# Performance work log

Hardware: AMD Instinct MI355X
Metric: run time of the kernel (lower is better)

## Reference

```python
import jax, jax.numpy as jnp
import numpy as np

N = 100000      # nodes per batched graph
E = 3200000     # edges per batched graph
G = 1024        # number of graphs in the batch
F_IN = 128
H = 64


def gcn_conv(x, src, dst, W, b, n):
    # PyG GCNConv: lin -> symmetric-normalized propagate (with self-loops) -> +bias
    xw = x @ W                                   # [n, out]
    deg = jnp.zeros((n,), x.dtype).at[dst].add(1.0) + 1.0   # A+I degree
    dinv = jax.lax.rsqrt(deg)                    # deg >= 1, safe
    norm = (dinv[src] * dinv[dst])[:, None]      # [E,1]
    agg = jax.ops.segment_sum(norm * xw[src], dst, num_segments=n)
    # self-loop contribution: dinv[i]^2 * xw[i]
    return agg + (dinv * dinv)[:, None] * xw + b


def mean_pool(h, batch, num_graphs):
    sums = jax.ops.segment_sum(h, batch, num_segments=num_graphs)
    cnt = jax.ops.segment_sum(jnp.ones((h.shape[0],), h.dtype), batch, num_segments=num_graphs)
    return sums / jnp.maximum(cnt, 1.0)[:, None]


def branch(x, edge_index, batch, W1, b1, W2, b2):
    src, dst = edge_index[0], edge_index[1]
    h = jax.nn.relu(gcn_conv(x, src, dst, W1, b1, x.shape[0]))
    h = jax.nn.relu(gcn_conv(h, src, dst, W2, b2, x.shape[0]))
    return mean_pool(h, batch, G)


def setup_inputs() -> dict:
    key = jax.random.key(0)
    ks = jax.random.split(key, 14)
    x1 = jax.random.normal(ks[0], (N, F_IN), jnp.float32)
    x2 = jax.random.normal(ks[1], (N, F_IN), jnp.float32)
    edge_index1 = jax.random.randint(ks[2], (2, E), 0, N, jnp.int32)
    edge_index2 = jax.random.randint(ks[3], (2, E), 0, N, jnp.int32)
    batch1 = jnp.sort(jax.random.randint(ks[4], (N,), 0, G, jnp.int32))
    batch2 = jnp.sort(jax.random.randint(ks[5], (N,), 0, G, jnp.int32))
    s = 1.0 / np.sqrt(F_IN)
    W1 = jax.random.uniform(ks[6], (F_IN, H), jnp.float32, -s, s)
    b1 = jnp.zeros((H,), jnp.float32)
    s2 = 1.0 / np.sqrt(H)
    W2 = jax.random.uniform(ks[7], (H, H), jnp.float32, -s2, s2)
    b2 = jnp.zeros((H,), jnp.float32)
    s3 = 1.0 / np.sqrt(3 * H)
    fc1_W = jax.random.uniform(ks[8], (3 * H, H), jnp.float32, -s3, s3)
    fc1_b = jax.random.uniform(ks[9], (H,), jnp.float32, -s3, s3)
    fc2_W = jax.random.uniform(ks[10], (H, 1), jnp.float32, -s2, s2)
    fc2_b = jax.random.uniform(ks[11], (1,), jnp.float32, -s2, s2)
    return {"x1": x1, "edge_index1": edge_index1, "batch1": batch1,
            "x2": x2, "edge_index2": edge_index2, "batch2": batch2,
            "W1": W1, "b1": b1, "W2": W2, "b2": b2,
            "fc1_W": fc1_W, "fc1_b": fc1_b, "fc2_W": fc2_W, "fc2_b": fc2_b}


def reference(x1, edge_index1, batch1, x2, edge_index2, batch2,
              W1, b1, W2, b2, fc1_W, fc1_b, fc2_W, fc2_b):
    emb1 = branch(x1, edge_index1, batch1, W1, b1, W2, b2)   # [G, 64]
    emb2 = branch(x2, edge_index2, batch2, W1, b1, W2, b2)   # [G, 64]
    combined = jnp.concatenate([emb1, emb2, jnp.abs(emb1 - emb2)], axis=1)  # [G, 192]
    out = jax.nn.relu(combined @ fc1_W + fc1_b)
    out = jax.nn.sigmoid(out @ fc2_W + fc2_b)
    return out.squeeze(-1)  # [G]
```

## Files before the change

kernel.cpp:

```cpp
#include <hip/hip_runtime.h>
#include <hip/hip_fp16.h>
#include <cstdint>


#define NBSH 8
#define CAPB 10240
#define SPLIT_T 512
#define SPLIT_EPT 28
#define SPLIT_CHUNK (SPLIT_T * SPLIT_EPT)

__device__ __forceinline__ float fatomic(float* p, float v) {
    return unsafeAtomicAdd(p, v);
}
__device__ __forceinline__ float bf2f(unsigned short u) {
    union { unsigned int i; float f; } c; c.i = ((unsigned int)u) << 16; return c.f;
}
__device__ __forceinline__ unsigned short f2bf(float f) {
    union { float f; unsigned int i; } c; c.f = f;
    const unsigned int b = c.i;
    return (unsigned short)((b + 0x7FFF + ((b >> 16) & 1)) >> 16);
}

#if defined(__has_builtin)
#if __has_builtin(__builtin_amdgcn_cvt_f32_fp8) && __has_builtin(__builtin_amdgcn_cvt_pk_fp8_f32)
#define HW_FP8 1
#endif
#endif

__device__ __forceinline__ float fp8dec(unsigned int b) {
#ifdef HW_FP8
    return __builtin_amdgcn_cvt_f32_fp8((int)b, 0);
#else
    const unsigned int mag = (b & 0x7Fu) << 20;
    const float f = __uint_as_float(mag) * __uint_as_float(0x7B800000u);
    const unsigned int r = __float_as_uint(f) | ((b & 0x80u) << 24);
    return __uint_as_float(r);
#endif
}

__device__ __forceinline__ unsigned char fp8enc(float x) {
#ifdef HW_FP8
    const int v = __builtin_amdgcn_cvt_pk_fp8_f32(x, x, 0, false);
    return (unsigned char)(v & 0xFF);
#else
    const unsigned short h = __half_as_ushort(__float2half(x));
    const unsigned int s = (unsigned int)(h >> 15) << 7;
    const int e = (h >> 10) & 0x1F;
    const unsigned int m = h & 0x3FFu;
    if (e == 31) return (unsigned char)(s | 0x7E);
    if (e == 0) return (unsigned char)s;
    int E = e - 15 + 7;
    if (E >= 16) return (unsigned char)(s | 0x7E);
    if (E <= 0) {
        const unsigned int M = 0x400u | m;
        const int r = 16 - e;
        const unsigned int q = (M + (1u << (r - 1)) - 1u + ((M >> r) & 1u)) >> r;
        return (unsigned char)(s | (q > 7u ? 8u : q));
    }
    unsigned int q = (m + 63u + ((m >> 7) & 1u)) >> 7;
    if (q == 8u) { q = 0u; ++E; if (E >= 16) return (unsigned char)(s | 0x7E); }
    return (unsigned char)(s | ((unsigned int)E << 3) | q);
#endif
}

__global__ __launch_bounds__(512) void k_split(const int* __restrict__ src,
                                               const int* __restrict__ dst,
                                               int* __restrict__ gcnt,
                                               int* __restrict__ colBkt,
                                               int E, int NBUK) {
    __shared__ int out[SPLIT_CHUNK];
    __shared__ int bs[513];
    __shared__ int aux[512];
    const int t = threadIdx.x;
    const int e0 = blockIdx.x * SPLIT_CHUNK;

    int pk[SPLIT_EPT];
    int bk[SPLIT_EPT];

    aux[t] = 0;
    __syncthreads();

#pragma unroll
    for (int k = 0; k < SPLIT_EPT; ++k) {
        const int e = e0 + t + SPLIT_T * k;
        if (e < E) {
            const int d = dst[e];
            const int s = src[e];
            const int b = d >> NBSH;
            pk[k] = (s << NBSH) | (d & ((1 << NBSH) - 1));
            bk[k] = b;
            atomicAdd(&aux[b], 1);
        } else {
            bk[k] = -1;
        }
    }
    __syncthreads();

    for (int off = 1; off < 512; off <<= 1) {
        const int u = (t >= off) ? aux[t - off] : 0;
        __syncthreads();
        aux[t] += u;
        __syncthreads();
    }
    bs[t + 1] = aux[t];
    if (t == 0) bs[0] = 0;
    __syncthreads();

    aux[t] = 0;
    __syncthreads();

#pragma unroll
    for (int k = 0; k < SPLIT_EPT; ++k) {
        if (bk[k] >= 0) {
            const int pos = bs[bk[k]] + atomicAdd(&aux[bk[k]], 1);
            out[pos] = pk[k];
        }
    }
    __syncthreads();

    if (t < NBUK) {
        const int L = bs[t + 1] - bs[t];
        aux[t] = (L > 0) ? atomicAdd(&gcnt[t], L) : 0;
    } else if (t < 512) {
        aux[t] = 0;
    }
    __syncthreads();

    const int wid = t >> 6, lane = t & 63;
    for (int b = wid; b < NBUK; b += 8) {
        const int L = bs[b + 1] - bs[b];
        if (L == 0) continue;
        const int gp = aux[b];
        const size_t rb = (size_t)b * CAPB;
        for (int k = lane; k < L; k += 64) {
            const int p = gp + k;
            if (p < CAPB) colBkt[rb + p] = out[bs[b] + k];
        }
    }
}

__global__ __launch_bounds__(512) void k_gscan(const int* __restrict__ gcnt,
                                               int* __restrict__ gbase,
                                               int* __restrict__ rowstart,
                                               int NBUK, int Nn) {
    __shared__ int sm[512];
    const int t = threadIdx.x;
    const int v = (t < NBUK) ? min(gcnt[t], CAPB) : 0;
    sm[t] = v;
    __syncthreads();
    for (int off = 1; off < 512; off <<= 1) {
        const int u = (t >= off) ? sm[t - off] : 0;
        __syncthreads();
        sm[t] += u;
        __syncthreads();
    }
    if (t < NBUK) gbase[t] = sm[t] - v;
    if (t == 511) rowstart[Nn] = sm[511];
}

__global__ __launch_bounds__(256) void k_bsort(const int* __restrict__ colBkt,
                                               const int* __restrict__ gcnt,
                                               const int* __restrict__ gbase,
                                               int* __restrict__ colN,
                                               int* __restrict__ rowstart,
                                               float* __restrict__ dinv,
                                               int Nn) {
    __shared__ int in[CAPB];
    __shared__ int lb[257];
    __shared__ int fill[256];
    const int b = blockIdx.x;
    const int t = threadIdx.x;
    const int L = min(gcnt[b], CAPB);
    const size_t rb = (size_t)b * CAPB;
    for (int k = t; k < L; k += 256) in[k] = colBkt[rb + k];
    fill[t] = 0;
    __syncthreads();
    for (int k = t; k < L; k += 256) atomicAdd(&fill[in[k] & 255], 1);
    __syncthreads();
    for (int off = 1; off < 256; off <<= 1) {
        const int u = (t >= off) ? fill[t - off] : 0;
        __syncthreads();
        fill[t] += u;
        __syncthreads();
    }
    lb[t + 1] = fill[t];
    if (t == 0) lb[0] = 0;
    __syncthreads();
    const int bb = gbase[b];
    const int node = (b << NBSH) + t;
    if (node < Nn) {
        rowstart[node] = bb + lb[t];
        dinv[node] = rsqrtf((float)(lb[t + 1] - lb[t]) + 1.0f);
    }
    fill[t] = 0;
    __syncthreads();
    for (int k = t; k < L; k += 256) {
        const int v = in[k];
        const int n = v & 255;
        const int pos = bb + lb[n] + atomicAdd(&fill[n], 1);
        colN[pos] = v >> NBSH;
    }
}

template <int K, bool BF16IN>
__global__ __launch_bounds__(256, 4) void k_mm(const void* __restrict__ Xv,
                                               const float* __restrict__ W,
                                               const float* __restrict__ dinv,
                                               unsigned char* __restrict__ Y, int n) {
    __shared__ float WL[K * 64];
    __shared__ float XT[32 * K];
    const int tid = threadIdx.x;
    for (int i = tid * 4; i < K * 64; i += 1024)
        *(float4*)&WL[i] = *(const float4*)&W[i];
    const int rowBase = blockIdx.x * 32;
    const int rows = min(32, n - rowBase);
    if (BF16IN) {
        const unsigned short* xs = (const unsigned short*)Xv + (size_t)rowBase * K;
        for (int i = tid * 4; i < rows * K; i += 1024) {
            const ushort4 u = *(const ushort4*)&xs[i];
            XT[i + 0] = bf2f(u.x); XT[i + 1] = bf2f(u.y);
            XT[i + 2] = bf2f(u.z); XT[i + 3] = bf2f(u.w);
        }
    } else {
        const float* xs = (const float*)Xv + (size_t)rowBase * K;
        for (int i = tid * 4; i < rows * K; i += 1024)
            *(float4*)&XT[i] = *(const float4*)&xs[i];
    }
    __syncthreads();
    const int colf = tid & 63;
    const int rg = tid >> 6;
    float acc[8] = {};
#pragma unroll 4
    for (int k4 = 0; k4 < K / 4; ++k4) {
        const float w0 = WL[(k4 * 4 + 0) * 64 + colf];
        const float w1 = WL[(k4 * 4 + 1) * 64 + colf];
        const float w2 = WL[(k4 * 4 + 2) * 64 + colf];
        const float w3 = WL[(k4 * 4 + 3) * 64 + colf];
#pragma unroll
        for (int r = 0; r < 8; ++r) {
            const float4 xv = *(const float4*)&XT[(rg * 8 + r) * K + k4 * 4];
            acc[r] += xv.x * w0 + xv.y * w1 + xv.z * w2 + xv.w * w3;
        }
    }
#pragma unroll
    for (int r = 0; r < 8; ++r) {
        const int row = rowBase + rg * 8 + r;
        if (row < n)
            __builtin_nontemporal_store(fp8enc(dinv[row] * acc[r]),
                                        &Y[(size_t)row * 64 + colf]);
    }
}

template <bool POOL>
__global__ __launch_bounds__(256) void k_agg(const int* __restrict__ colN,
                                             const int* __restrict__ rowstart,
                                             const float* __restrict__ dinv,
                                             const unsigned char* __restrict__ XW8,
                                             const float* __restrict__ bias,
                                             unsigned short* __restrict__ Hout,
                                             const int* __restrict__ batch,
                                             float* __restrict__ emb,
                                             float* __restrict__ cnt, int Nn) {
    const int lane = threadIdx.x & 63;
    const int wid = (blockIdx.x * blockDim.x + threadIdx.x) >> 6;
    const int nw = (gridDim.x * blockDim.x) >> 6;
    const float bl = bias[lane];
    for (int i = wid; i < Nn; i += nw) {
        const int s = rowstart[i], e = rowstart[i + 1];
        float acc = 0.0f;
        int j = s;
        for (; j + 16 <= e; j += 16) {
            int c[16];
#pragma unroll
            for (int q = 0; q < 16; ++q) c[q] = __builtin_nontemporal_load(&colN[j + q]);
            unsigned int b[16];
#pragma unroll
            for (int q = 0; q < 16; ++q) b[q] = XW8[(size_t)c[q] * 64 + lane];
            float t0 = 0.f, t1 = 0.f;
#pragma unroll
            for (int q = 0; q < 8; ++q) t0 += fp8dec(b[q]);
#pragma unroll
            for (int q = 8; q < 16; ++q) t1 += fp8dec(b[q]);
            acc += t0 + t1;
        }
        for (; j + 4 <= e; j += 4) {
            const int c0 = __builtin_nontemporal_load(&colN[j + 0]);
            const int c1 = __builtin_nontemporal_load(&colN[j + 1]);
            const int c2 = __builtin_nontemporal_load(&colN[j + 2]);
            const int c3 = __builtin_nontemporal_load(&colN[j + 3]);
            const float a0 = fp8dec(XW8[(size_t)c0 * 64 + lane]);
            const float a1 = fp8dec(XW8[(size_t)c1 * 64 + lane]);
            const float a2 = fp8dec(XW8[(size_t)c2 * 64 + lane]);
            const float a3 = fp8dec(XW8[(size_t)c3 * 64 + lane]);
            acc += (a0 + a1) + (a2 + a3);
        }
        for (; j < e; ++j) {
            const int c0 = __builtin_nontemporal_load(&colN[j]);
            acc += fp8dec(XW8[(size_t)c0 * 64 + lane]);
        }
        const float di = dinv[i];
        const float self = fp8dec(XW8[(size_t)i * 64 + lane]);
        const float v = fmaxf(di * (acc + self) + bl, 0.0f);
        if (POOL) {
            const int g = batch[i];
            fatomic(&emb[(size_t)g * 64 + lane], v);
            if (lane == 0) fatomic(&cnt[g], 1.0f);
        } else {
            __builtin_nontemporal_store(f2bf(v), &Hout[(size_t)i * 64 + lane]);
        }
    }
}

__global__ __launch_bounds__(64) void k_head(const float* __restrict__ emb1, const float* __restrict__ cnt1,
                                             const float* __restrict__ emb2, const float* __restrict__ cnt2,
                                             const float* __restrict__ fc1W, const float* __restrict__ fc1b,
                                             const float* __restrict__ fc2W, const float* __restrict__ fc2b,
                                             float* __restrict__ out) {
    const int g = blockIdx.x;
    const int lane = threadIdx.x;
    __shared__ float comb[192];
    const float c1 = fmaxf(cnt1[g], 1.0f), c2 = fmaxf(cnt2[g], 1.0f);
    const float e1 = emb1[g * 64 + lane] / c1;
    const float e2 = emb2[g * 64 + lane] / c2;
    comb[lane] = e1;
    comb[64 + lane] = e2;
    comb[128 + lane] = fabsf(e1 - e2);
    __syncthreads();
    float acc = fc1b[lane];
    for (int k = 0; k < 192; ++k) acc += comb[k] * fc1W[k * 64 + lane];
    const float o1 = fmaxf(acc, 0.0f);
    float p = o1 * fc2W[lane];
#pragma unroll
    for (int off = 32; off > 0; off >>= 1) p += __shfl_xor(p, off);
    if (lane == 0) out[g] = 1.0f / (1.0f + expf(-(p + fc2b[0])));
}

extern "C" void kernel_launch(void* const* d_in, const int* in_sizes, int n_in,
                              void* d_out, int out_size, void* d_ws, size_t ws_size,
                              hipStream_t stream) {
    const float* x1   = (const float*)d_in[0];
    const int*   ei1  = (const int*)d_in[1];
    const int*   bt1  = (const int*)d_in[2];
    const float* x2   = (const float*)d_in[3];
    const int*   ei2  = (const int*)d_in[4];
    const int*   bt2  = (const int*)d_in[5];
    const float* W1   = (const float*)d_in[6];
    const float* bb1  = (const float*)d_in[7];
    const float* W2   = (const float*)d_in[8];
    const float* bb2  = (const float*)d_in[9];
    const float* fc1W = (const float*)d_in[10];
    const float* fc1b = (const float*)d_in[11];
    const float* fc2W = (const float*)d_in[12];
    const float* fc2b = (const float*)d_in[13];
    float* out = (float*)d_out;

    const int N = in_sizes[0] / 128;
    const int E = in_sizes[1] / 2;
    const int G = out_size;
    const int NBUK = (N + 255) >> NBSH;
    const int nchunks = (E + SPLIT_CHUNK - 1) / SPLIT_CHUNK;

    char* base = (char*)d_ws;
    size_t off = 0;
    auto carve = [&](size_t bytes) {
        void* p = base + off;
        off = (off + bytes + 15) & ~(size_t)15;
        return p;
    };
    float* dinv   = (float*)carve((size_t)N * 4);
    float* emb1   = (float*)carve((size_t)G * 64 * 4);
    float* cnt1   = (float*)carve((size_t)G * 4);
    float* emb2   = (float*)carve((size_t)G * 64 * 4);
    float* cnt2   = (float*)carve((size_t)G * 4);
    int* rowstart = (int*)carve((size_t)(N + 1) * 4);
    int* gcnt     = (int*)carve(512 * 4);
    int* gbase    = (int*)carve(512 * 4);
    int* colBkt   = (int*)carve((size_t)NBUK * CAPB * 4);
    int* colN     = (int*)carve((size_t)E * 4);
    unsigned char* XW8 = (unsigned char*)carve((size_t)N * 64);
    unsigned short* H1 = (unsigned short*)colBkt;

    const int mmGrid = (N + 31) / 32;

    for (int br = 0; br < 2; ++br) {
        const float* X = br ? x2 : x1;
        const int* ei  = br ? ei2 : ei1;
        const int* bt  = br ? bt2 : bt1;
        float* emb = br ? emb2 : emb1;
        float* cnt = br ? cnt2 : cnt1;
        const int* srcp = ei;
        const int* dstp = ei + E;

        hipMemsetAsync(gcnt, 0, 512 * 4, stream);
        k_split<<<nchunks, SPLIT_T, 0, stream>>>(srcp, dstp, gcnt, colBkt, E, NBUK);
        k_gscan<<<1, 512, 0, stream>>>(gcnt, gbase, rowstart, NBUK, N);
        k_bsort<<<NBUK, 256, 0, stream>>>(colBkt, gcnt, gbase, colN, rowstart, dinv, N);

        k_mm<128, false><<<mmGrid, 256, 0, stream>>>(X, W1, dinv, XW8, N);
        k_agg<false><<<2048, 256, 0, stream>>>(colN, rowstart, dinv, XW8, bb1,
                                               H1, nullptr, nullptr, nullptr, N);
        k_mm<64, true><<<mmGrid, 256, 0, stream>>>(H1, W2, dinv, XW8, N);
        hipMemsetAsync(emb, 0, (size_t)(G * 64 + G) * 4, stream);
        k_agg<true><<<2048, 256, 0, stream>>>(colN, rowstart, dinv, XW8, bb2,
                                              nullptr, bt, emb, cnt, N);
    }
    k_head<<<G, 64, 0, stream>>>(emb1, cnt1, emb2, cnt2, fc1W, fc1b, fc2W, fc2b, out);
}
```

Before: 816.5 us.

## Gather fp8 rows as 4-byte words across 4 edges per wave in aggregation

```diff
diff --git a/kernel.cpp b/kernel.cpp
--- a/kernel.cpp
+++ b/kernel.cpp
@@ -27,16 +27,17 @@
 #endif
 #endif
 
-__device__ __forceinline__ float fp8dec(unsigned int b) {
-#ifdef HW_FP8
-    return __builtin_amdgcn_cvt_f32_fp8((int)b, 0);
-#else
+__device__ __forceinline__ float fp8dec_sw(unsigned int b) {
     const unsigned int mag = (b & 0x7Fu) << 20;
     const float f = __uint_as_float(mag) * __uint_as_float(0x7B800000u);
     const unsigned int r = __float_as_uint(f) | ((b & 0x80u) << 24);
     return __uint_as_float(r);
+}
+#ifdef HW_FP8
+#define FP8D(v, k) __builtin_amdgcn_cvt_f32_fp8((int)(v), (k))
+#else
+#define FP8D(v, k) fp8dec_sw(((v) >> ((k) * 8)) & 255u)
 #endif
-}
 
 __device__ __forceinline__ unsigned char fp8enc(float x) {
 #ifdef HW_FP8
@@ -262,51 +263,63 @@
                                              float* __restrict__ emb,
                                              float* __restrict__ cnt, int Nn) {
     const int lane = threadIdx.x & 63;
+    const int c16 = lane & 15;
+    const int jj = lane >> 4;
+    const int boff = c16 * 4;
     const int wid = (blockIdx.x * blockDim.x + threadIdx.x) >> 6;
     const int nw = (gridDim.x * blockDim.x) >> 6;
-    const float bl = bias[lane];
+    const float bl0 = bias[boff + 0], bl1 = bias[boff + 1];
+    const float bl2 = bias[boff + 2], bl3 = bias[boff + 3];
     for (int i = wid; i < Nn; i += nw) {
         const int s = rowstart[i], e = rowstart[i + 1];
-        float acc = 0.0f;
+        float a0 = 0.f, a1 = 0.f, a2 = 0.f, a3 = 0.f;
         int j = s;
         for (; j + 16 <= e; j += 16) {
-            int c[16];
-#pragma unroll
-            for (int q = 0; q < 16; ++q) c[q] = __builtin_nontemporal_load(&colN[j + q]);
-            unsigned int b[16];
-#pragma unroll
-            for (int q = 0; q < 16; ++q) b[q] = XW8[(size_t)c[q] * 64 + lane];
-            float t0 = 0.f, t1 = 0.f;
-#pragma unroll
-            for (int q = 0; q < 8; ++q) t0 += fp8dec(b[q]);
-#pragma unroll
-            for (int q = 8; q < 16; ++q) t1 += fp8dec(b[q]);
-            acc += t0 + t1;
-        }
-        for (; j + 4 <= e; j += 4) {
-            const int c0 = __builtin_nontemporal_load(&colN[j + 0]);
-            const int c1 = __builtin_nontemporal_load(&colN[j + 1]);
-            const int c2 = __builtin_nontemporal_load(&colN[j + 2]);
-            const int c3 = __builtin_nontemporal_load(&colN[j + 3]);
-            const float a0 = fp8dec(XW8[(size_t)c0 * 64 + lane]);
-            const float a1 = fp8dec(XW8[(size_t)c1 * 64 + lane]);
-            const float a2 = fp8dec(XW8[(size_t)c2 * 64 + lane]);
-            const float a3 = fp8dec(XW8[(size_t)c3 * 64 + lane]);
-            acc += (a0 + a1) + (a2 + a3);
-        }
-        for (; j < e; ++j) {
-            const int c0 = __builtin_nontemporal_load(&colN[j]);
-            acc += fp8dec(XW8[(size_t)c0 * 64 + lane]);
-        }
-        const float di = dinv[i];
-        const float self = fp8dec(XW8[(size_t)i * 64 + lane]);
-        const float v = fmaxf(di * (acc + self) + bl, 0.0f);
-        if (POOL) {
-            const int g = batch[i];
-            fatomic(&emb[(size_t)g * 64 + lane], v);
-            if (lane == 0) fatomic(&cnt[g], 1.0f);
-        } else {
-            __builtin_nontemporal_store(f2bf(v), &Hout[(size_t)i * 64 + lane]);
+            const int cA = colN[j + jj];
+            const int cB = colN[j + 4 + jj];
+            const int cC = colN[j + 8 + jj];
+            const int cD = colN[j + 12 + jj];
+            const unsigned int vA = *(const unsigned int*)&XW8[(size_t)cA * 64 + boff];
+            const unsigned int vB = *(const unsigned int*)&XW8[(size_t)cB * 64 + boff];
+            const unsigned int vC = *(const unsigned int*)&XW8[(size_t)cC * 64 + boff];
+            const unsigned int vD = *(const unsigned int*)&XW8[(size_t)cD * 64 + boff];
+            a0 += (FP8D(vA, 0) + FP8D(vB, 0)) + (FP8D(vC, 0) + FP8D(vD, 0));
+            a1 += (FP8D(vA, 1) + FP8D(vB, 1)) + (FP8D(vC, 1) + FP8D(vD, 1));
+            a2 += (FP8D(vA, 2) + FP8D(vB, 2)) + (FP8D(vC, 2) + FP8D(vD, 2));
+            a3 += (FP8D(vA, 3) + FP8D(vB, 3)) + (FP8D(vC, 3) + FP8D(vD, 3));
+        }
+        for (; j < e; j += 4) {
+            if (j + jj < e) {
+                const int cA = colN[j + jj];
+                const unsigned int vA = *(const unsigned int*)&XW8[(size_t)cA * 64 + boff];
+                a0 += FP8D(vA, 0);
+                a1 += FP8D(vA, 1);
+                a2 += FP8D(vA, 2);
+                a3 += FP8D(vA, 3);
+            }
+        }
+        a0 += __shfl_xor(a0, 16); a0 += __shfl_xor(a0, 32);
+        a1 += __shfl_xor(a1, 16); a1 += __shfl_xor(a1, 32);
+        a2 += __shfl_xor(a2, 16); a2 += __shfl_xor(a2, 32);
+        a3 += __shfl_xor(a3, 16); a3 += __shfl_xor(a3, 32);
+        if (jj == 0) {
+            const float di = dinv[i];
+            const unsigned int sv = *(const unsigned int*)&XW8[(size_t)i * 64 + boff];
+            const float v0 = fmaxf(di * (a0 + FP8D(sv, 0)) + bl0, 0.0f);
+            const float v1 = fmaxf(di * (a1 + FP8D(sv, 1)) + bl1, 0.0f);
+            const float v2 = fmaxf(di * (a2 + FP8D(sv, 2)) + bl2, 0.0f);
+            const float v3 = fmaxf(di * (a3 + FP8D(sv, 3)) + bl3, 0.0f);
+            if (POOL) {
+                const int g = batch[i];
+                float* ep = &emb[(size_t)g * 64 + boff];
+                fatomic(ep + 0, v0); fatomic(ep + 1, v1);
+                fatomic(ep + 2, v2); fatomic(ep + 3, v3);
+                if (c16 == 0) fatomic(&cnt[g], 1.0f);
+            } else {
+                ushort4 o;
+                o.x = f2bf(v0); o.y = f2bf(v1); o.z = f2bf(v2); o.w = f2bf(v3);
+                *(ushort4*)&Hout[(size_t)i * 64 + boff] = o;
+            }
         }
     }
 }
```

Result: slower. 848.8 us (+4.0%).
